# Kernel tuning notes

Measured on AMD Instinct MI355X. Metric: run time of the kernel, lower is better.

The kernel has to match this reference:

```python
import jax, jax.numpy as jnp
import numpy as np

B, C, H, W = 8, 256, 64, 64
NUM_HEADS = 8
HEAD_DIM = C // NUM_HEADS  # 32
KSIZE = 3
DILATIONS = [1, 2, 3, 4]
SCALE = HEAD_DIM ** -0.5


def _unfold(x, k, dil):
    # x: (B, d, H, W) -> (B, d, k*k, H, W), matching torch nn.Unfold with
    # padding = dil*(k-1)//2 and channel-major patch ordering.
    p = dil * (k - 1) // 2
    xp = jnp.pad(x, ((0, 0), (0, 0), (p, p), (p, p)))
    h, w = x.shape[2], x.shape[3]
    patches = [xp[:, :, i * dil:i * dil + h, j * dil:j * dil + w]
               for i in range(k) for j in range(k)]
    return jnp.stack(patches, axis=2)


def setup_inputs() -> dict:
    key = jax.random.key(0)
    k1, k2, k3, k4, k5 = jax.random.split(key, 5)
    x = jax.random.normal(k1, (B, C, H, W), dtype=jnp.float32)
    w_qkv = jax.random.normal(k2, (3 * C, C), dtype=jnp.float32) * 0.02
    b_qkv = jnp.zeros((3 * C,), dtype=jnp.float32)
    w_proj = jax.random.normal(k3, (C, C), dtype=jnp.float32) * 0.02
    b_proj = jnp.zeros((C,), dtype=jnp.float32)
    return {"x": x, "w_qkv": w_qkv, "b_qkv": b_qkv,
            "w_proj": w_proj, "b_proj": b_proj}


def reference(x, w_qkv, b_qkv, w_proj, b_proj):
    b, c, h, w = x.shape
    # 1x1 conv qkv projection
    qkv = jnp.einsum('bchw,oc->bohw', x, w_qkv) + b_qkv[None, :, None, None]
    qkv = qkv.reshape(b, 3, NUM_HEADS, HEAD_DIM, h, w)
    outs = []
    for hd in range(NUM_HEADS):  # small fixed loop; heads structurally distinct (dilation)
        dil = DILATIONS[hd % len(DILATIONS)]
        q = qkv[:, 0, hd]   # (B, d, H, W)
        k_ = qkv[:, 1, hd]
        v = qkv[:, 2, hd]
        kk = _unfold(k_, KSIZE, dil)  # (B, d, K2, H, W)
        vv = _unfold(v, KSIZE, dil)
        attn = jax.nn.softmax(
            jnp.einsum('bdhw,bdKhw->bKhw', q, kk) * SCALE, axis=1)
        outs.append(jnp.einsum('bKhw,bdKhw->bdhw', attn, vv))
    # torch.stack(dim=1).reshape(B,C,H,W) => head-major channel concat
    out = jnp.concatenate(outs, axis=1)  # (B, C, H, W)
    out = jnp.einsum('bchw,oc->bohw', out, w_proj) + b_proj[None, :, None, None]
    return out
```

## Files before the change

### kernel.cpp

```cpp
#include <hip/hip_runtime.h>
#include <cstdint>

typedef unsigned short ushortT;
typedef __attribute__((ext_vector_type(8))) short short8;
typedef __attribute__((ext_vector_type(8))) unsigned short ushort8v;
typedef __attribute__((ext_vector_type(4))) float float4v;

#define ATT_SCALE 0.17677669529663687f

__device__ inline float bf2f(unsigned short u) {
    union { unsigned int i; float f; } x; x.i = ((unsigned int)u) << 16; return x.f;
}
__device__ inline unsigned short f2bf(float f) {
    union { float f; unsigned int i; } x; x.f = f;
    unsigned int i = x.i;
    i += 0x7fffu + ((i >> 16) & 1u);
    return (unsigned short)(i >> 16);
}

__device__ inline void gld_lds16(const ushortT* g, ushortT* l) {
    __builtin_amdgcn_global_load_lds((const __attribute__((address_space(1))) void*)g,
                                     (__attribute__((address_space(3))) void*)l, 16, 0, 0);
}

__global__ __launch_bounds__(256) void transpose_cp(const float* __restrict__ x,
                                                    ushortT* __restrict__ xT,
                                                    const float* __restrict__ w_qkv,
                                                    const float* __restrict__ w_proj,
                                                    const float* __restrict__ b_qkv,
                                                    const float* __restrict__ b_proj,
                                                    ushortT* __restrict__ wqkvB,
                                                    ushortT* __restrict__ wprojB,
                                                    float* __restrict__ bqF,
                                                    float* __restrict__ bpF) {
    __shared__ __align__(16) ushortT tile[64][65];
    const int b  = blockIdx.z;
    const int c0 = blockIdx.x * 64;
    const int p0 = blockIdx.y * 64;
    const int t  = threadIdx.x;

    {
        int flat = blockIdx.x + 4 * blockIdx.y + 256 * blockIdx.z;
        if (flat < 1028) {
            int i = flat * 256 + t;
            if (i < 196608) {
                wqkvB[i] = f2bf(w_qkv[i]);
            } else if (i < 262144) {
                wprojB[i - 196608] = f2bf(w_proj[i - 196608]);
            } else if (i < 262912) {
                bqF[i - 262144] = b_qkv[i - 262144];
            } else if (i < 263168) {
                bpF[i - 262912] = b_proj[i - 262912];
            }
        }
    }

    const float* xb = x + (size_t)b * 256 * 4096;
#pragma unroll
    for (int it = 0; it < 4; it++) {
        int id  = t + it * 256;
        int row = id >> 4;
        int c4  = (id & 15) * 4;
        float4 v = *(const float4*)(xb + (size_t)(c0 + row) * 4096 + p0 + c4);
        tile[row][c4 + 0] = f2bf(v.x);
        tile[row][c4 + 1] = f2bf(v.y);
        tile[row][c4 + 2] = f2bf(v.z);
        tile[row][c4 + 3] = f2bf(v.w);
    }
    __syncthreads();
    ushortT* xTb = xT + (size_t)b * 4096 * 256;
#pragma unroll
    for (int it = 0; it < 2; it++) {
        int id   = t + it * 256;
        int prow = id >> 3;
        int cc   = (id & 7) * 8;
        ushort8v v;
#pragma unroll
        for (int j = 0; j < 8; j++) v[j] = tile[cc + j][prow];
        *(ushort8v*)(xTb + (size_t)(p0 + prow) * 256 + c0 + cc) = v;
    }
}

__global__ __launch_bounds__(256) void gemm_bt(const ushortT* __restrict__ A,
                                               const ushortT* __restrict__ Bt, long long sBb,
                                               int ldb, int bHeadMajor,
                                               void* __restrict__ D, long long sDb,
                                               int ldd, int dHeadMajor, int outF32,
                                               const float* __restrict__ bias, int biasAlongM,
                                               int K, int swizzleMode) {
    __shared__ __align__(16) ushortT pool[12288];

    int mIdx, nIdx, bz;
    {
        int id = blockIdx.x;
        int r  = id & 7;
        int j  = id >> 3;
        if (swizzleMode == 0) {
            mIdx = r * 64 + j / 6;
            nIdx = j % 6;
            bz   = 0;
        } else {
            mIdx = j & 3;
            int pp = r * 32 + (j >> 2);
            bz   = pp >> 5;
            nIdx = pp & 31;
        }
    }
    const int n0 = nIdx * 128;
    const int m0 = mIdx * 64;
    Bt += (size_t)bz * sBb;

    const int t    = threadIdx.x;
    const int wv   = t >> 6;
    const int lane = t & 63;
    const int lm   = lane & 15;
    const int quad = lane >> 4;
    const int wm   = wv & 1;
    const int wn   = wv >> 1;

    ushortT* Als = pool;
    ushortT* Bls = pool + 4096;

    float4v acc[2][4];
#pragma unroll
    for (int i = 0; i < 2; i++)
#pragma unroll
        for (int j = 0; j < 4; j++) { float4v z = {0.f, 0.f, 0.f, 0.f}; acc[i][j] = z; }

    const int nkt = K >> 6;
    for (int kt = 0; kt < nkt; ++kt) {
        __syncthreads();
#pragma unroll
        for (int j = 0; j < 2; j++) {
            int cid = wv * 128 + j * 64 + lane;
            int row = cid >> 3;
            int s   = cid & 7;
            int gc  = s ^ (row & 7);
            gld_lds16(A + (size_t)(m0 + row) * K + kt * 64 + gc * 8,
                      Als + (size_t)cid * 8);
        }
#pragma unroll
        for (int j = 0; j < 4; j++) {
            int cid = wv * 256 + j * 64 + lane;
            int row = cid >> 3;
            int s   = cid & 7;
            int gc  = s ^ (row & 7);
            const ushortT* gb = bHeadMajor
                ? Bt + ((size_t)(kt * 2 + (gc >> 2)) * 32768 + (n0 + row)) * 32 + (gc & 3) * 8
                : Bt + (size_t)(n0 + row) * ldb + kt * 64 + gc * 8;
            gld_lds16(gb, Bls + (size_t)cid * 8);
        }
        asm volatile("s_waitcnt vmcnt(0)" ::: "memory");
        __syncthreads();

#pragma unroll
        for (int g = 0; g < 2; g++) {
            short8 af[2], bfr[4];
#pragma unroll
            for (int i = 0; i < 2; i++) {
                int r = wm * 32 + i * 16 + lm;
                int slot = (g * 4 + quad) ^ (r & 7);
                af[i] = *(const short8*)&Als[r * 64 + slot * 8];
            }
#pragma unroll
            for (int j = 0; j < 4; j++) {
                int r = wn * 64 + j * 16 + lm;
                int slot = (g * 4 + quad) ^ (r & 7);
                bfr[j] = *(const short8*)&Bls[r * 64 + slot * 8];
            }
#pragma unroll
            for (int i = 0; i < 2; i++)
#pragma unroll
                for (int j = 0; j < 4; j++)
                    acc[i][j] = __builtin_amdgcn_mfma_f32_16x16x32_bf16(af[i], bfr[j], acc[i][j], 0, 0, 0);
        }
    }

    if (dHeadMajor) {
        __syncthreads();
#pragma unroll
        for (int i = 0; i < 2; i++) {
#pragma unroll
            for (int j = 0; j < 4; j++) {
                int c = wn * 64 + j * 16 + lm;
#pragma unroll
                for (int rg = 0; rg < 4; rg++) {
                    int r = wm * 32 + i * 16 + quad * 4 + rg;
                    float v = acc[i][j][rg] + bias[biasAlongM ? (m0 + r) : (n0 + c)];
                    int chunk = (c >> 3) ^ (r & 7);
                    pool[r * 128 + chunk * 8 + (c & 7)] = f2bf(v);
                }
            }
        }
        __syncthreads();
        ushortT* Dh = (ushortT*)D + (size_t)bz * sDb;
#pragma unroll
        for (int g = 0; g < 4; g++) {
            ushortT* base = Dh + ((size_t)((n0 >> 5) + g) * 32768 + m0) * 32;
            int r  = t >> 2;
            int cb = t & 3;
            int pch = (g * 4 + cb) ^ (r & 7);
            ushort8v v = *(const ushort8v*)&pool[r * 128 + pch * 8];
            *(ushort8v*)(base + r * 32 + cb * 8) = v;
        }
    } else if (outF32) {
        float* poolF = (float*)pool;
        float* Df = (float*)D + (size_t)bz * sDb;
#pragma unroll
        for (int pass = 0; pass < 2; pass++) {
            __syncthreads();
            if (wn == pass) {
#pragma unroll
                for (int i = 0; i < 2; i++) {
#pragma unroll
                    for (int j = 0; j < 4; j++) {
                        int c = j * 16 + lm;
                        #pragma unroll
                        for (int rg = 0; rg < 4; rg++) {
                            int r64 = wm * 32 + i * 16 + quad * 4 + rg;
                            float v = acc[i][j][rg] +
                                      bias[biasAlongM ? (m0 + r64) : (n0 + pass * 64 + c)];
                            int phys = (c + 4 * r64) & 63;
                            poolF[r64 * 64 + phys] = v;
                        }
                    }
                }
            }
            __syncthreads();
#pragma unroll
            for (int it = 0; it < 4; it++) {
                int id  = it * 256 + t;
                int r64 = id >> 4;
                int c   = (id & 15) * 4;
                int phys = (c + 4 * r64) & 63;
                float4v v = *(const float4v*)&poolF[r64 * 64 + phys];
                *(float4v*)&Df[(size_t)(m0 + r64) * ldd + n0 + pass * 64 + c] = v;
            }
        }
    } else {
        ushortT* Dh = (ushortT*)D + (size_t)bz * sDb;
#pragma unroll
        for (int i = 0; i < 2; i++) {
            int r0 = m0 + wm * 32 + i * 16 + quad * 4;
#pragma unroll
            for (int j = 0; j < 4; j++) {
                int c = n0 + wn * 64 + j * 16 + lm;
#pragma unroll
                for (int rg = 0; rg < 4; rg++) {
                    int r = r0 + rg;
                    float v = acc[i][j][rg] + bias[biasAlongM ? r : c];
                    Dh[(size_t)r * ldd + c] = f2bf(v);
                }
            }
        }
    }
}

__global__ __launch_bounds__(256, 8) void attn_k(ushortT* qkv) {
    const int gt      = blockIdx.x * 256 + threadIdx.x;
    const int quarter = gt & 3;
    const int pix     = gt >> 2;
    const int hd      = pix >> 15;
    const int rem     = pix & 32767;
    const int b       = rem >> 12;
    const int p       = rem & 4095;
    const int h       = p >> 6;
    const int w       = p & 63;
    const int dil     = (hd & 3) + 1;
    const int c0      = quarter * 8;

    ushortT*       qp    = qkv + ((size_t)hd * 32768 + (size_t)b * 4096 + p) * 32 + c0;
    const ushortT* kbase = qkv + ((size_t)(8  + hd) * 32768 + (size_t)b * 4096) * 32 + c0;
    const ushortT* vbase = qkv + ((size_t)(16 + hd) * 32768 + (size_t)b * 4096) * 32 + c0;

    float q[8];
    {
        ushort8v v = *(const ushort8v*)qp;
#pragma unroll
        for (int j = 0; j < 8; j++) q[j] = bf2f(v[j]);
    }

    float lgt[9];
    int   nb[9];
    unsigned vmask = 0;
#pragma unroll
    for (int ii = 0; ii < 3; ii++) {
#pragma unroll
        for (int jj = 0; jj < 3; jj++) {
            int idx = ii * 3 + jj;
            int hh = h + (ii - 1) * dil;
            int ww = w + (jj - 1) * dil;
            bool ok = ((unsigned)hh < 64u) && ((unsigned)ww < 64u);
            int pp = (hh << 6) + ww;
            nb[idx] = pp;
            float l = 0.f;
            if (ok) {
                vmask |= (1u << idx);
                ushort8v v = *(const ushort8v*)(kbase + (size_t)pp * 32);
#pragma unroll
                for (int j = 0; j < 8; j++) l += q[j] * bf2f(v[j]);
            }
            lgt[idx] = l;
        }
    }
#pragma unroll
    for (int i = 0; i < 9; i++) {
        float l = lgt[i];
        l += __shfl_xor(l, 1);
        l += __shfl_xor(l, 2);
        lgt[i] = l * ATT_SCALE;
    }

    float mx = lgt[0];
#pragma unroll
    for (int i = 1; i < 9; i++) mx = fmaxf(mx, lgt[i]);
    float e[9], s = 0.f;
#pragma unroll
    for (int i = 0; i < 9; i++) { e[i] = __expf(lgt[i] - mx); s += e[i]; }
    const float inv = 1.f / s;

    float acc[8];
#pragma unroll
    for (int d = 0; d < 8; d++) acc[d] = 0.f;
#pragma unroll
    for (int idx = 0; idx < 9; idx++) {
        if ((vmask >> idx) & 1u) {
            float pj = e[idx] * inv;
            ushort8v v = *(const ushort8v*)(vbase + (size_t)nb[idx] * 32);
#pragma unroll
            for (int j = 0; j < 8; j++) acc[j] += pj * bf2f(v[j]);
        }
    }

    {
        ushort8v v;
#pragma unroll
        for (int j = 0; j < 8; j++) v[j] = f2bf(acc[j]);
        *(ushort8v*)qp = v;
    }
}

extern "C" void kernel_launch(void* const* d_in, const int* in_sizes, int n_in,
                              void* d_out, int out_size, void* d_ws, size_t ws_size,
                              hipStream_t stream) {
    const float* x      = (const float*)d_in[0];
    const float* w_qkv  = (const float*)d_in[1];
    const float* b_qkv  = (const float*)d_in[2];
    const float* w_proj = (const float*)d_in[3];
    const float* b_proj = (const float*)d_in[4];

    char* ws = (char*)d_ws;
    float*   bqF    = (float*)(ws + 256);
    float*   bpF    = (float*)(ws + 3328);
    ushortT* wqkvB  = (ushortT*)(ws + 4352);
    ushortT* wprojB = (ushortT*)(ws + 397568);
    ushortT* qkv    = (ushortT*)(ws + 528640);
    ushortT* xT     = (ushortT*)d_out;

    transpose_cp<<<dim3(4, 64, 8), 256, 0, stream>>>(x, xT, w_qkv, w_proj, b_qkv, b_proj,
                                                     wqkvB, wprojB, bqF, bpF);

    gemm_bt<<<dim3(3072), 256, 0, stream>>>(xT, wqkvB, 0, 256, 0,
                                            qkv, 0, 0, 1, 0,
                                            bqF, 0, 256, 0);

    attn_k<<<dim3(4096), 256, 0, stream>>>(qkv);

    gemm_bt<<<dim3(1024), 256, 0, stream>>>(wprojB, qkv, (long long)4096 * 32, 0, 1,
                                            d_out, (long long)256 * 4096, 4096, 0, 1,
                                            bpF, 1, 256, 1);
}
```

Measured before the change: 149.7 us.

## Stage K/V neighbor rows in LDS for dilated neighborhood attention

Each 256-thread block covers one image row of one head. It now loads the three needed K and V rows (offset by dilation) into shared memory with global_load_lds, then reads the 3x3 neighbors from LDS instead of issuing scattered global loads. This cuts repeated global and L2 traffic for overlapping neighborhoods. In exchange it adds 24KB of LDS per block, a full wait plus barrier, and drops the occupancy hint from the launch bounds.

```diff
diff --git a/kernel.cpp b/kernel.cpp
--- a/kernel.cpp
+++ b/kernel.cpp
@@ -256,8 +256,12 @@
     }
 }
 
-__global__ __launch_bounds__(256, 8) void attn_k(ushortT* qkv) {
-    const int gt      = blockIdx.x * 256 + threadIdx.x;
+__global__ __launch_bounds__(256) void attn_k(ushortT* qkv) {
+    __shared__ __align__(16) ushortT kls[6144];
+    __shared__ __align__(16) ushortT vls[6144];
+
+    const int tid     = threadIdx.x;
+    const int gt      = blockIdx.x * 256 + tid;
     const int quarter = gt & 3;
     const int pix     = gt >> 2;
     const int hd      = pix >> 15;
@@ -269,9 +273,28 @@
     const int dil     = (hd & 3) + 1;
     const int c0      = quarter * 8;
 
+    const int wv   = tid >> 6;
+    const int lane = tid & 63;
+
     ushortT*       qp    = qkv + ((size_t)hd * 32768 + (size_t)b * 4096 + p) * 32 + c0;
-    const ushortT* kbase = qkv + ((size_t)(8  + hd) * 32768 + (size_t)b * 4096) * 32 + c0;
-    const ushortT* vbase = qkv + ((size_t)(16 + hd) * 32768 + (size_t)b * 4096) * 32 + c0;
+    const ushortT* kfull = qkv + ((size_t)(8  + hd) * 32768 + (size_t)b * 4096) * 32;
+    const ushortT* vfull = qkv + ((size_t)(16 + hd) * 32768 + (size_t)b * 4096) * 32;
+
+#pragma unroll
+    for (int i = 0; i < 6; i++) {
+        int s    = wv * 6 + i;
+        int part = (s >= 12);
+        int r3   = (s % 12) >> 2;
+        int qs   = s & 3;
+        int hh   = h + (r3 - 1) * dil;
+        if ((unsigned)hh < 64u) {
+            const ushortT* src = (part ? vfull : kls == nullptr ? kfull : kfull)
+                                 + (size_t)hh * 2048 + qs * 512 + lane * 8;
+            if (part) src = vfull + (size_t)hh * 2048 + qs * 512 + lane * 8;
+            ushortT* dst = (part ? vls : kls) + r3 * 2048 + qs * 512 + lane * 8;
+            gld_lds16(src, dst);
+        }
+    }
 
     float q[8];
     {
@@ -280,8 +303,10 @@
         for (int j = 0; j < 8; j++) q[j] = bf2f(v[j]);
     }
 
+    asm volatile("s_waitcnt vmcnt(0)" ::: "memory");
+    __syncthreads();
+
     float lgt[9];
-    int   nb[9];
     unsigned vmask = 0;
 #pragma unroll
     for (int ii = 0; ii < 3; ii++) {
@@ -291,12 +316,10 @@
             int hh = h + (ii - 1) * dil;
             int ww = w + (jj - 1) * dil;
             bool ok = ((unsigned)hh < 64u) && ((unsigned)ww < 64u);
-            int pp = (hh << 6) + ww;
-            nb[idx] = pp;
             float l = 0.f;
             if (ok) {
                 vmask |= (1u << idx);
-                ushort8v v = *(const ushort8v*)(kbase + (size_t)pp * 32);
+                ushort8v v = *(const ushort8v*)&kls[ii * 2048 + ww * 32 + c0];
 #pragma unroll
                 for (int j = 0; j < 8; j++) l += q[j] * bf2f(v[j]);
             }
@@ -323,12 +346,17 @@
 #pragma unroll
     for (int d = 0; d < 8; d++) acc[d] = 0.f;
 #pragma unroll
-    for (int idx = 0; idx < 9; idx++) {
-        if ((vmask >> idx) & 1u) {
-            float pj = e[idx] * inv;
-            ushort8v v = *(const ushort8v*)(vbase + (size_t)nb[idx] * 32);
-#pragma unroll
-            for (int j = 0; j < 8; j++) acc[j] += pj * bf2f(v[j]);
+    for (int ii = 0; ii < 3; ii++) {
+#pragma unroll
+        for (int jj = 0; jj < 3; jj++) {
+            int idx = ii * 3 + jj;
+            if ((vmask >> idx) & 1u) {
+                int ww = w + (jj - 1) * dil;
+                float pj = e[idx] * inv;
+                ushort8v v = *(const ushort8v*)&vls[ii * 2048 + ww * 32 + c0];
+#pragma unroll
+                for (int j = 0; j < 8; j++) acc[j] += pj * bf2f(v[j]);
+            }
         }
     }
 
```

New measurement: 146.3 us. -2.3%, faster.
